# Performance work log

Hardware: AMD Instinct MI355X
Metric: run time of the kernel (lower is better)

## Reference

```python
import jax, jax.numpy as jnp
import numpy as np

B, V, T, F, H = 32, 16, 64, 64, 512
NBINS = 36  # 360 / delta (delta_cog = delta_rb = 10)
OUT = 4     # output_size


def setup_inputs() -> dict:
    key = jax.random.key(0)
    ks = jax.random.split(key, 12)
    s = 1.0 / np.sqrt(H)
    return {
        'sequence': jax.random.normal(ks[0], (B, V, T, F), jnp.float32),
        'dist_matrix': jax.random.uniform(ks[1], (B, V, T, V), jnp.float32),
        'rb_matrix': jax.random.randint(ks[2], (B, V, T, V), 0, NBINS).astype(jnp.int32),
        'cog_matrix': jax.random.randint(ks[3], (B, V, T, V), 0, NBINS).astype(jnp.int32),
        'seq_mask': jnp.ones((B, V, T), jnp.float32),
        'maxval': jax.random.uniform(ks[4], (B, F), jnp.float32) + 1.0,
        'minval': jax.random.uniform(ks[5], (B, F), jnp.float32),
        # per-vessel LSTMCell params (PyTorch gate order i,f,g,o stacked along 4H)
        'W_ih': jax.random.normal(ks[6], (V, 4 * H, F), jnp.float32) * s,
        'W_hh': jax.random.normal(ks[7], (V, 4 * H, H), jnp.float32) * s,
        'b_ih': jnp.zeros((V, 4 * H), jnp.float32),
        'b_hh': jnp.zeros((V, 4 * H), jnp.float32),
        # hardwired attention domain table [360/delta_cog, 360/delta_rb]
        'domain': jax.random.normal(ks[8], (NBINS, NBINS), jnp.float32),
        # per-vessel softAttention linear (2H -> H)
        'soft_W': jax.random.normal(ks[9], (V, H, 2 * H), jnp.float32) * s,
        'soft_b': jnp.zeros((V, H), jnp.float32),
        # shared output linear (H -> F)
        'out_W': jax.random.normal(ks[10], (F, H), jnp.float32) * s,
        'out_b': jnp.zeros((F,), jnp.float32),
    }


def _forward(sequence, dist_matrix, rb_matrix, cog_matrix, seq_mask, maxval, minval,
             W_ih, W_hh, b_ih, b_hh, domain, soft_W, soft_b, out_W, out_b):
    B_, V_, T_, F_ = sequence.shape
    H_ = W_hh.shape[-1]

    def hardwired(h, r, d, m, cg):
        # h: [B,V,H]; r,d,cg: [B,V,V]; m: [B,V]
        mul1 = m[:, :, None] * m[:, None, :]
        mul2 = domain[cg, r]
        w = jax.nn.relu(mul2 - d) * mul1
        w = w / jax.lax.stop_gradient(jnp.max(w))  # torch: weights /= weights.data.max()
        return jnp.einsum('bvw,bwh->bvh', w, h)

    def lstm_step(x, h, c):
        # vectorized over V independent LSTMCells
        g = (jnp.einsum('bvf,vgf->bvg', x, W_ih)
             + jnp.einsum('bvh,vgh->bvg', h, W_hh) + b_ih + b_hh)
        i, f, gg, o = jnp.split(g, 4, axis=-1)
        c_new = jax.nn.sigmoid(f) * c + jax.nn.sigmoid(i) * jnp.tanh(gg)
        h_new = jax.nn.sigmoid(o) * jnp.tanh(c_new)
        return h_new, c_new

    h0 = jnp.zeros((B_, V_, H_), sequence.dtype)
    c0 = jnp.zeros((B_, V_, H_), sequence.dtype)
    xs = (jnp.moveaxis(sequence, 2, 0), jnp.moveaxis(rb_matrix, 2, 0),
          jnp.moveaxis(dist_matrix, 2, 0), jnp.moveaxis(seq_mask, 2, 0),
          jnp.moveaxis(cog_matrix, 2, 0))

    def enc_step(carry, xt):
        h, c = carry
        x, r, d, m, cg = xt
        wh = hardwired(h, r, d, m, cg)
        h, c = lstm_step(x, wh, c)
        return (h, c), h

    (h, c), enc = jax.lax.scan(enc_step, (h0, c0), xs)
    enc = jnp.moveaxis(enc, 0, 2)  # encodedInput [B,V,T,H]

    # decoder, prediction step i=0 (prediction_length=1)
    wh = hardwired(h, rb_matrix[:, :, -1], dist_matrix[:, :, -1],
                   seq_mask[:, :, -1], cog_matrix[:, :, -1])
    # get_previous_sequence: denormalize under no_grad
    prev = jax.lax.stop_gradient(
        sequence[:, :, -1] * (maxval - minval)[:, None, :] + minval[:, None, :])
    h, c = lstm_step(prev, wh, c)

    # per-vessel softAttention
    score = jnp.einsum('bvth,bvh->bvt', enc, h)
    alpha = jax.nn.softmax(score * seq_mask, axis=-1)
    ctx = jnp.einsum('bvt,bvth->bvh', alpha, enc)
    # faithful to torch.stack((ctx, h)).view(B, 2H) memory-reinterpret per vessel
    z = jnp.moveaxis(jnp.stack([ctx, h], axis=0), 2, 0).reshape(V_, B_, 2 * H_)
    h = jnp.moveaxis(
        jnp.tanh(jnp.einsum('vbk,vhk->vbh', z, soft_W) + soft_b[:, None, :]), 0, 1)

    out = jax.nn.relu(jnp.einsum('bvh,fh->bvf', h, out_W) + out_b)
    return out[:, :, None, :OUT]  # [B, V, prediction_length=1, output_size]


def reference(sequence, dist_matrix, rb_matrix, cog_matrix, seq_mask, maxval, minval,
              W_ih, W_hh, b_ih, b_hh, domain, soft_W, soft_b, out_W, out_b,
              maxVessels=V):
    return _forward(sequence, dist_matrix, rb_matrix, cog_matrix, seq_mask,
                    maxval, minval, W_ih, W_hh, b_ih, b_hh, domain,
                    soft_W, soft_b, out_W, out_b)
```

## Files before the change

### kernel.cpp

```cpp
#include <hip/hip_runtime.h>
#include <math.h>

#define B 32
#define V 16
#define T 64
#define F 64
#define H 512
#define NB 36
#define G4H 2048

typedef unsigned short u16;
typedef unsigned long long ull;
typedef __attribute__((ext_vector_type(8))) short bf16x8;
typedef __attribute__((ext_vector_type(4))) float f32x4;

#define OFF_H0     0
#define OFF_H1     262144
#define OFF_C      524288
#define OFF_CNT    786432
#define OFF_WALL   819200
#define OFF_CTX    819200
#define OFF_HSOFT  1081344
#define OFF_WMAX   1343488
#define OFF_WHSTG  1343552
#define OFF_SEQSTG 1605696
#define OFF_WSTG   2670656
#define OFF_ENC    12107840

#define WHP 262144
#define WLDS_BYTES 147456

__device__ __forceinline__ float sigmoidf_(float x) { return 1.0f / (1.0f + __expf(-x)); }

__device__ __forceinline__ u16 f2bf(float f) {
    union { float f; unsigned u; } x; x.f = f;
    unsigned r = x.u + 0x7FFF + ((x.u >> 16) & 1);
    return (u16)(r >> 16);
}
__device__ __forceinline__ float bf2f(u16 u) {
    union { unsigned i; float f; } x; x.i = ((unsigned)u) << 16;
    return x.f;
}
__device__ __forceinline__ f32x4 mfma16(bf16x8 a, bf16x8 b, f32x4 c) {
    return __builtin_amdgcn_mfma_f32_16x16x32_bf16(a, b, c, 0, 0, 0);
}
__device__ __forceinline__ bf16x8 mk_bf16x8(ull lo, ull hi) {
    union { ull u[2]; bf16x8 v; } x; x.u[0] = lo; x.u[1] = hi; return x.v;
}
__device__ __forceinline__ bf16x8 mk_bf16x8q(uint4 q) {
    union { uint4 q; bf16x8 v; } x; x.q = q; return x.v;
}

__device__ __forceinline__ ull ld_agent(const ull* p) {
    return __hip_atomic_load((ull*)p, __ATOMIC_RELAXED, __HIP_MEMORY_SCOPE_AGENT);
}
__device__ __forceinline__ void st_agent(ull* p, ull x) {
    __hip_atomic_store(p, x, __ATOMIC_RELAXED, __HIP_MEMORY_SCOPE_AGENT);
}
__device__ __forceinline__ void st_agent_f(float* p, float x) {
    __hip_atomic_store(p, x, __ATOMIC_RELAXED, __HIP_MEMORY_SCOPE_AGENT);
}
__device__ __forceinline__ void st_agent_u16(u16* p, u16 x) {
    __hip_atomic_store(p, x, __ATOMIC_RELAXED, __HIP_MEMORY_SCOPE_AGENT);
}
__device__ __forceinline__ void st_agent_u32(unsigned* p, unsigned x) {
    __hip_atomic_store(p, x, __ATOMIC_RELAXED, __HIP_MEMORY_SCOPE_AGENT);
}
__device__ __forceinline__ unsigned ld_agent_u32(const unsigned* p) {
    return __hip_atomic_load((unsigned*)p, __ATOMIC_RELAXED, __HIP_MEMORY_SCOPE_AGENT);
}

#define NZB 3200
#define NHW 64
#define NWC 4608
#define NSS 1040
__global__ __launch_bounds__(256) void k_prep(
    float* __restrict__ ws,
    const float* __restrict__ dist, const int* __restrict__ rb,
    const int* __restrict__ cog, const float* __restrict__ mask,
    const float* __restrict__ domain, float* __restrict__ w_all,
    float* __restrict__ wmax_all,
    const float* __restrict__ W_ih, const float* __restrict__ W_hh,
    u16* __restrict__ Wstg,
    const float* __restrict__ seq, const float* __restrict__ maxval,
    const float* __restrict__ minval, u16* __restrict__ seqstg) {
    __shared__ float red[256];
    int bid = blockIdx.x;
    int tid = threadIdx.x;

    if (bid < NZB) {
        ws[bid * 256 + tid] = 0.0f;
        return;
    }
    if (bid < NZB + NHW) {
        int t = bid - NZB;
        float lmax = 0.0f;
        for (int idx = tid; idx < B * V * V; idx += 256) {
            int b = idx >> 8;
            int rem = idx & 255;
            int i = rem >> 4, j = rem & 15;
            int base = ((b * V + i) * T + t) * V + j;
            float val = domain[cog[base] * NB + rb[base]] - dist[base];
            val = val > 0.0f ? val : 0.0f;
            val *= mask[(b * V + i) * T + t] * mask[(b * V + j) * T + t];
            w_all[t * (B * V * V) + idx] = val;
            lmax = fmaxf(lmax, val);
        }
        red[tid] = lmax;
        __syncthreads();
        for (int s = 128; s > 0; s >>= 1) {
            if (tid < s) red[tid] = fmaxf(red[tid], red[tid + s]);
            __syncthreads();
        }
        if (tid == 0) wmax_all[t] = red[0];
        return;
    }
    if (bid < NZB + NHW + NWC) {
        int idx = bid - (NZB + NHW);
        int v = idx / 288, hk = (idx / 18) & 15, ks = idx % 18;
#pragma unroll
        for (int s = 0; s < 2; ++s) {
            int slot = tid + s * 256;
            int nt = slot >> 6, lane = slot & 63;
            int g = nt >> 1, hh = nt & 1;
            int col = g * H + hk * 32 + hh * 16 + (lane & 15);
            int k = ks * 32 + ((lane >> 4) << 3);
            const float* src = (k < F) ? &W_ih[(v * G4H + col) * F + k]
                                       : &W_hh[(v * G4H + col) * H + (k - F)];
            float4 x0 = *(const float4*)src;
            float4 x1 = *(const float4*)(src + 4);
            union { u16 u[8]; uint4 q; } pk;
            pk.u[0] = f2bf(x0.x); pk.u[1] = f2bf(x0.y); pk.u[2] = f2bf(x0.z); pk.u[3] = f2bf(x0.w);
            pk.u[4] = f2bf(x1.x); pk.u[5] = f2bf(x1.y); pk.u[6] = f2bf(x1.z); pk.u[7] = f2bf(x1.w);
            *(uint4*)&Wstg[(size_t)((((v * 16 + hk) * 18 + ks) * 8 + nt) * 64 + lane) * 8] = pk.q;
        }
        return;
    }
    {
        int idx = bid - (NZB + NHW + NWC);
        int v = idx / 65, t = idx % 65;
        int mt = tid >> 7, ks = (tid >> 6) & 1, lane = tid & 63;
        int b = mt * 16 + (lane & 15);
        int f = ks * 32 + ((lane >> 4) << 3);
        union { u16 u[8]; uint4 q; } pk;
        if (t < T) {
            const float* sp = &seq[((b * V + v) * T + t) * F + f];
            float4 x0 = *(const float4*)sp, x1 = *(const float4*)(sp + 4);
            pk.u[0] = f2bf(x0.x); pk.u[1] = f2bf(x0.y); pk.u[2] = f2bf(x0.z); pk.u[3] = f2bf(x0.w);
            pk.u[4] = f2bf(x1.x); pk.u[5] = f2bf(x1.y); pk.u[6] = f2bf(x1.z); pk.u[7] = f2bf(x1.w);
        } else {
            const float* sp = &seq[((b * V + v) * T + (T - 1)) * F + f];
            float4 x0 = *(const float4*)sp, x1 = *(const float4*)(sp + 4);
            float4 mx0 = *(const float4*)&maxval[b * F + f], mx1 = *(const float4*)&maxval[b * F + f + 4];
            float4 mn0 = *(const float4*)&minval[b * F + f], mn1 = *(const float4*)&minval[b * F + f + 4];
            pk.u[0] = f2bf(x0.x * (mx0.x - mn0.x) + mn0.x);
            pk.u[1] = f2bf(x0.y * (mx0.y - mn0.y) + mn0.y);
            pk.u[2] = f2bf(x0.z * (mx0.z - mn0.z) + mn0.z);
            pk.u[3] = f2bf(x0.w * (mx0.w - mn0.w) + mn0.w);
            pk.u[4] = f2bf(x1.x * (mx1.x - mn1.x) + mn1.x);
            pk.u[5] = f2bf(x1.y * (mx1.y - mn1.y) + mn1.y);
            pk.u[6] = f2bf(x1.z * (mx1.z - mn1.z) + mn1.z);
            pk.u[7] = f2bf(x1.w * (mx1.w - mn1.w) + mn1.w);
        }
        *(uint4*)&seqstg[(((size_t)(t * 16 + v)) * 4 + mt * 2 + ks) * 512 + lane * 8] = pk.q;
    }
}

__global__ __launch_bounds__(256) void k_main(
    const u16* __restrict__ seqstg, const u16* __restrict__ Wstg,
    const float* __restrict__ w_all, const float* __restrict__ wmax_all,
    const float* __restrict__ b_ih, const float* __restrict__ b_hh,
    float* __restrict__ h0buf, float* __restrict__ h1buf,
    float* __restrict__ c, u16* __restrict__ enc, u16* __restrict__ whstg,
    unsigned* __restrict__ bar,
    const float* __restrict__ mask, const float* __restrict__ soft_W,
    const float* __restrict__ soft_b, const float* __restrict__ out_W,
    const float* __restrict__ out_b, float* __restrict__ ctx,
    float* __restrict__ hsoft, float* __restrict__ out) {
    extern __shared__ u16 Wlds[];
    __shared__ float hs[H];
    __shared__ float scal[2 * T];
    __shared__ float sA[32][36];
    __shared__ float sW2[32][36];

    int bid = blockIdx.x;
    int v = bid & 15, hk = bid >> 4;
    int tid = threadIdx.x;

    {
        const uint4* wsrc = (const uint4*)(Wstg + (size_t)((v * 16 + hk) * 18) * 4096);
        uint4* wdst = (uint4*)Wlds;
        for (int i = tid; i < 9216; i += 256) wdst[i] = wsrc[i];
    }

    int lane = tid & 63, wvi = tid >> 6;
    int mtw = wvi & 1, hh = wvi >> 1;
    int col = hk * 32 + hh * 16 + (lane & 15);
    int q4 = (lane >> 4) << 2;
    float bi = b_ih[v * G4H + col] + b_hh[v * G4H + col];
    float bf_ = b_ih[v * G4H + H + col] + b_hh[v * G4H + H + col];
    float bg_ = b_ih[v * G4H + 2 * H + col] + b_hh[v * G4H + 2 * H + col];
    float bo = b_ih[v * G4H + 3 * H + col] + b_hh[v * G4H + 3 * H + col];

    unsigned* aslot = bar + (v * 16 + hk) * 16;
    unsigned* bslot = bar + (256 + hk * 16 + v) * 16;
    unsigned* apoll = bar + (v * 16 + (tid & 15)) * 16;
    unsigned* bpoll = bar + (256 + hk * 16 + (tid & 15)) * 16;

    int a_b = tid >> 3;
    int a_cq = tid & 7;
    const int wh_idx = ((((v * 2 + (a_b >> 4)) * 16 + hk) * 64 +
                         (((a_cq >> 1) << 4) + (a_b & 15))) * 8 + (a_cq & 1) * 4);

    __syncthreads();

    for (int t = 0; t <= T; ++t) {
        int par = t & 1;
        int tm = t < T ? t : (T - 1);
        const float* hin = (t & 1) ? h0buf : h1buf;
        float* hout = (t & 1) ? h1buf : h0buf;

        uint4 s0 = *(const uint4*)&seqstg[(((size_t)(t * 16 + v)) * 4 + mtw * 2 + 0) * 512 + lane * 8];
        uint4 s1 = *(const uint4*)&seqstg[(((size_t)(t * 16 + v)) * 4 + mtw * 2 + 1) * 512 + lane * 8];
        float inv = 1.0f / wmax_all[tm];
        const float* wrow = &w_all[(size_t)tm * (B * V * V) + (a_b * V + v) * V];
        float4 wr0 = *(const float4*)(wrow);
        float4 wr1 = *(const float4*)(wrow + 4);
        float4 wr2 = *(const float4*)(wrow + 8);
        float4 wr3 = *(const float4*)(wrow + 12);
        float cprev[4];
#pragma unroll
        for (int r = 0; r < 4; ++r)
            cprev[r] = c[((mtw * 16 + q4 + r) * V + v) * H + col];

        f32x4 acc[4];
        acc[0][0] = bi;  acc[0][1] = bi;  acc[0][2] = bi;  acc[0][3] = bi;
        acc[1][0] = bf_; acc[1][1] = bf_; acc[1][2] = bf_; acc[1][3] = bf_;
        acc[2][0] = bg_; acc[2][1] = bg_; acc[2][2] = bg_; acc[2][3] = bg_;
        acc[3][0] = bo;  acc[3][1] = bo;  acc[3][2] = bo;  acc[3][3] = bo;
        {
            bf16x8 a0f = mk_bf16x8q(s0);
            bf16x8 a1f = mk_bf16x8q(s1);
#pragma unroll
            for (int g = 0; g < 4; ++g)
                acc[g] = mfma16(a0f, *(const bf16x8*)&Wlds[(0 * 8 + (g * 2 + hh)) * 512 + lane * 8], acc[g]);
#pragma unroll
            for (int g = 0; g < 4; ++g)
                acc[g] = mfma16(a1f, *(const bf16x8*)&Wlds[(1 * 8 + (g * 2 + hh)) * 512 + lane * 8], acc[g]);
        }

        if (t > 0) {
            if (tid < 16) {
                while (ld_agent_u32(bpoll) < (unsigned)t) __builtin_amdgcn_s_sleep(1);
            }
            __syncthreads();
        }

        {
            const ull* hb = (const ull*)&hin[(a_b * V) * H + hk * 32 + a_cq * 4];
            float a0 = 0.f, a1 = 0.f, a2 = 0.f, a3 = 0.f;
            const float wj[16] = {wr0.x, wr0.y, wr0.z, wr0.w, wr1.x, wr1.y, wr1.z, wr1.w,
                                  wr2.x, wr2.y, wr2.z, wr2.w, wr3.x, wr3.y, wr3.z, wr3.w};
#pragma unroll
            for (int j = 0; j < 16; ++j) {
                ull lo = ld_agent(hb + (size_t)j * (H / 2));
                ull hi = ld_agent(hb + (size_t)j * (H / 2) + 1);
                union { ull u; float f[2]; } u0, u1;
                u0.u = lo; u1.u = hi;
                a0 = fmaf(wj[j], u0.f[0], a0);
                a1 = fmaf(wj[j], u0.f[1], a1);
                a2 = fmaf(wj[j], u1.f[0], a2);
                a3 = fmaf(wj[j], u1.f[1], a3);
            }
            union { u16 u[4]; ull q; } pk;
            pk.u[0] = f2bf(a0 * inv); pk.u[1] = f2bf(a1 * inv);
            pk.u[2] = f2bf(a2 * inv); pk.u[3] = f2bf(a3 * inv);
            st_agent((ull*)&whstg[par * WHP + wh_idx], pk.q);
        }
        __syncthreads();
        if (tid == 0) st_agent_u32(aslot, (unsigned)(t + 1));

        if (tid < 16) {
            while (ld_agent_u32(apoll) < (unsigned)(t + 1)) __builtin_amdgcn_s_sleep(1);
        }
        __syncthreads();

        bf16x8 afr[16];
#pragma unroll
        for (int ksw = 0; ksw < 16; ++ksw) {
            const ull* src = (const ull*)&whstg[par * WHP + (((v * 2 + mtw) * 16 + ksw) * 64 + lane) * 8];
            ull lo = ld_agent(src), hi = ld_agent(src + 1);
            afr[ksw] = mk_bf16x8(lo, hi);
        }
#pragma unroll
        for (int ks = 0; ks < 16; ++ks) {
#pragma unroll
            for (int g = 0; g < 4; ++g) {
                bf16x8 wfr = *(const bf16x8*)&Wlds[((ks + 2) * 8 + (g * 2 + hh)) * 512 + lane * 8];
                acc[g] = mfma16(afr[ks], wfr, acc[g]);
            }
        }

        float cnv[4], hnv[4];
#pragma unroll
        for (int r = 0; r < 4; ++r) {
            float gi = acc[0][r];
            float gf = acc[1][r];
            float gg = acc[2][r];
            float go = acc[3][r];
            cnv[r] = sigmoidf_(gf) * cprev[r] + sigmoidf_(gi) * tanhf(gg);
            hnv[r] = sigmoidf_(go) * tanhf(cnv[r]);
            int b = mtw * 16 + q4 + r;
            st_agent_f(&hout[(b * V + v) * H + col], hnv[r]);
        }
        if (t < T) {
            __syncthreads();
            if (tid == 0) st_agent_u32(bslot, (unsigned)(t + 1));
        }

#pragma unroll
        for (int r = 0; r < 4; ++r) {
            int b = mtw * 16 + q4 + r;
            c[(b * V + v) * H + col] = cnv[r];
            if (t < T) st_agent_u16(&enc[((size_t)(b * V + v) * T + t) * H + col], f2bf(hnv[r]));
        }
    }

    __syncthreads();
    if (tid == 0) st_agent_u32(bar + (512 + bid) * 16, 1u);
    {
        const unsigned* rs = bar + (512 + tid) * 16;
        while (ld_agent_u32(rs) < 1u) __builtin_amdgcn_s_sleep(1);
    }
    __syncthreads();

    for (int u = 0; u < 2; ++u) {
        int ab = (bid >> 4) + u * 16;
        int av = bid & 15;
        const u16* encb = enc + ((size_t)(ab * V + av) * T) * H;
        {
            ull x = ld_agent((const ull*)(h0buf + (ab * V + av) * H) + tid);
            union { ull u; float f[2]; } q; q.u = x;
            hs[tid * 2] = q.f[0]; hs[tid * 2 + 1] = q.f[1];
        }
        __syncthreads();
        for (int tt = wvi; tt < T; tt += 4) {
            const ull* ep = (const ull*)(encb + tt * H + lane * 8);
            ull lo = ld_agent(ep), hi = ld_agent(ep + 1);
            union { ull u; u16 s[4]; } x0, x1; x0.u = lo; x1.u = hi;
            const float* hq = &hs[lane * 8];
            float p = bf2f(x0.s[0]) * hq[0] + bf2f(x0.s[1]) * hq[1]
                    + bf2f(x0.s[2]) * hq[2] + bf2f(x0.s[3]) * hq[3]
                    + bf2f(x1.s[0]) * hq[4] + bf2f(x1.s[1]) * hq[5]
                    + bf2f(x1.s[2]) * hq[6] + bf2f(x1.s[3]) * hq[7];
            for (int off = 32; off; off >>= 1) p += __shfl_down(p, off, 64);
            if (lane == 0) scal[tt] = p;
        }
        __syncthreads();
        if (tid < 64) {
            float m_t = mask[(ab * V + av) * T + tid];
            float s = scal[tid] * m_t;
            float mx = s;
            for (int off = 32; off; off >>= 1) mx = fmaxf(mx, __shfl_xor(mx, off, 64));
            float e = __expf(s - mx);
            float sum = e;
            for (int off = 32; off; off >>= 1) sum += __shfl_xor(sum, off, 64);
            scal[T + tid] = e / sum;
        }
        __syncthreads();
        if (tid < 128) {
            float a0 = 0.f, a1 = 0.f, a2 = 0.f, a3 = 0.f;
            for (int tt = 0; tt < T; ++tt) {
                ull x = ld_agent((const ull*)(encb + tt * H + tid * 4));
                union { ull u; u16 s[4]; } q; q.u = x;
                float al = scal[T + tt];
                a0 = fmaf(al, bf2f(q.s[0]), a0);
                a1 = fmaf(al, bf2f(q.s[1]), a1);
                a2 = fmaf(al, bf2f(q.s[2]), a2);
                a3 = fmaf(al, bf2f(q.s[3]), a3);
            }
            float* cp = ctx + (ab * V + av) * H + tid * 4;
            union { float f[2]; ull u; } q0, q1;
            q0.f[0] = a0; q0.f[1] = a1; q1.f[0] = a2; q1.f[1] = a3;
            st_agent((ull*)cp, q0.u);
            st_agent((ull*)cp + 1, q1.u);
        }
        __syncthreads();
    }
    __syncthreads();
    if (tid == 0) st_agent_u32(bar + (768 + bid) * 16, 1u);

    {
        int sv = bid & 15;
        int h0 = (bid >> 4) * 32;
        if (tid < 16) {
            const unsigned* cs = bar + (768 + tid * 16 + sv) * 16;
            while (ld_agent_u32(cs) < 1u) __builtin_amdgcn_s_sleep(1);
        }
        __syncthreads();

        int cg = tid & 31, rg = tid >> 5;
        float* sAf = &sA[0][0];
        float* sWf = &sW2[0][0];
        float accs[4] = {0.f, 0.f, 0.f, 0.f};
        int arow = tid >> 3, akq = tid & 7;
        float4 areg, wreg;
        {
            int k = akq * 4;
            const float* src = (arow < 16) ? ctx : h0buf;
            int bsrc = 2 * (arow & 15) + (k >= H ? 1 : 0);
            const float* sp = &src[(bsrc * V + sv) * H + (k & (H - 1))];
            ull l0 = ld_agent((const ull*)sp), l1 = ld_agent((const ull*)sp + 1);
            union { ull u[2]; float4 f; } q; q.u[0] = l0; q.u[1] = l1;
            areg = q.f;
            wreg = *(const float4*)&soft_W[(sv * H + h0 + arow) * (2 * H) + k];
        }
        for (int kc = 0; kc < 2 * H; kc += 32) {
            __syncthreads();
            *(float4*)&sAf[arow * 36 + akq * 4] = areg;
            *(float4*)&sWf[arow * 36 + akq * 4] = wreg;
            __syncthreads();
            if (kc + 32 < 2 * H) {
                int k = kc + 32 + akq * 4;
                const float* src = (arow < 16) ? ctx : h0buf;
                int bsrc = 2 * (arow & 15) + (k >= H ? 1 : 0);
                const float* sp = &src[(bsrc * V + sv) * H + (k & (H - 1))];
                ull l0 = ld_agent((const ull*)sp), l1 = ld_agent((const ull*)sp + 1);
                union { ull u[2]; float4 f; } q; q.u[0] = l0; q.u[1] = l1;
                areg = q.f;
                wreg = *(const float4*)&soft_W[(sv * H + h0 + arow) * (2 * H) + kc + 32 + akq * 4];
            }
#pragma unroll
            for (int k4 = 0; k4 < 8; ++k4) {
                float4 wv = *(const float4*)&sWf[cg * 36 + k4 * 4];
                float4 a0 = *(const float4*)&sAf[(rg * 4 + 0) * 36 + k4 * 4];
                float4 a1 = *(const float4*)&sAf[(rg * 4 + 1) * 36 + k4 * 4];
                float4 a2 = *(const float4*)&sAf[(rg * 4 + 2) * 36 + k4 * 4];
                float4 a3 = *(const float4*)&sAf[(rg * 4 + 3) * 36 + k4 * 4];
                accs[0] += a0.x * wv.x + a0.y * wv.y + a0.z * wv.z + a0.w * wv.w;
                accs[1] += a1.x * wv.x + a1.y * wv.y + a1.z * wv.z + a1.w * wv.w;
                accs[2] += a2.x * wv.x + a2.y * wv.y + a2.z * wv.z + a2.w * wv.w;
                accs[3] += a3.x * wv.x + a3.y * wv.y + a3.z * wv.z + a3.w * wv.w;
            }
        }
        float bb = soft_b[sv * H + h0 + cg];
#pragma unroll
        for (int r = 0; r < 4; ++r) {
            int row = rg * 4 + r;
            st_agent_f(&hsoft[(row * V + sv) * H + h0 + cg], tanhf(accs[r] + bb));
        }
    }
    __syncthreads();
    if (tid == 0) st_agent_u32(bar + (1024 + bid) * 16, 1u);

    {
        int ov = bid & 15;
        if (tid < 16) {
            const unsigned* ss = bar + (1024 + tid * 16 + ov) * 16;
            while (ld_agent_u32(ss) < 1u) __builtin_amdgcn_s_sleep(1);
        }
        __syncthreads();
        if (wvi < 2) {
            int ob = (bid >> 4) + wvi * 16;
            const float* hbp = hsoft + (ob * V + ov) * H + lane * 8;
            ull q0 = ld_agent((const ull*)hbp);
            ull q1 = ld_agent((const ull*)hbp + 1);
            ull q2 = ld_agent((const ull*)hbp + 2);
            ull q3 = ld_agent((const ull*)hbp + 3);
            union { ull u[4]; float f[8]; } hv;
            hv.u[0] = q0; hv.u[1] = q1; hv.u[2] = q2; hv.u[3] = q3;
            float p[4] = {0.f, 0.f, 0.f, 0.f};
#pragma unroll
            for (int o = 0; o < 4; ++o) {
                const float* wp = &out_W[o * H + lane * 8];
#pragma unroll
                for (int j = 0; j < 8; ++j) p[o] += hv.f[j] * wp[j];
            }
#pragma unroll
            for (int o = 0; o < 4; ++o) {
                float s = p[o];
                for (int off = 32; off; off >>= 1) s += __shfl_down(s, off, 64);
                if (lane == 0) {
                    float val = s + out_b[o];
                    out[(ob * V + ov) * 4 + o] = val > 0.0f ? val : 0.0f;
                }
            }
        }
    }
}

extern "C" void kernel_launch(void* const* d_in, const int* in_sizes, int n_in,
                              void* d_out, int out_size, void* d_ws, size_t ws_size,
                              hipStream_t stream) {
    const float* seq = (const float*)d_in[0];
    const float* dist = (const float*)d_in[1];
    const int* rb = (const int*)d_in[2];
    const int* cog = (const int*)d_in[3];
    const float* mask = (const float*)d_in[4];
    const float* maxval = (const float*)d_in[5];
    const float* minval = (const float*)d_in[6];
    const float* W_ih = (const float*)d_in[7];
    const float* W_hh = (const float*)d_in[8];
    const float* b_ih = (const float*)d_in[9];
    const float* b_hh = (const float*)d_in[10];
    const float* domain = (const float*)d_in[11];
    const float* soft_W = (const float*)d_in[12];
    const float* soft_b = (const float*)d_in[13];
    const float* out_W = (const float*)d_in[14];
    const float* out_b = (const float*)d_in[15];

    float* ws = (float*)d_ws;
    float* h0buf = ws + OFF_H0;
    float* h1buf = ws + OFF_H1;
    float* c = ws + OFF_C;
    unsigned* bar = (unsigned*)(ws + OFF_CNT);
    float* w_all = ws + OFF_WALL;
    float* ctx = ws + OFF_CTX;
    float* hsoft = ws + OFF_HSOFT;
    float* wmax_all = ws + OFF_WMAX;
    u16* whstg = (u16*)(ws + OFF_WHSTG);
    u16* seqstg = (u16*)(ws + OFF_SEQSTG);
    u16* Wstg = (u16*)(ws + OFF_WSTG);
    u16* enc = (u16*)(ws + OFF_ENC);

    (void)hipFuncSetAttribute((const void*)k_main,
                              hipFuncAttributeMaxDynamicSharedMemorySize, WLDS_BYTES);

    k_prep<<<NZB + NHW + NWC + NSS, 256, 0, stream>>>(
        ws, dist, rb, cog, mask, domain, w_all, wmax_all,
        W_ih, W_hh, Wstg, seq, maxval, minval, seqstg);

    k_main<<<256, 256, WLDS_BYTES, stream>>>(seqstg, Wstg, w_all, wmax_all,
                                             b_ih, b_hh, h0buf, h1buf, c, enc,
                                             whstg, bar, mask, soft_W, soft_b,
                                             out_W, out_b, ctx, hsoft,
                                             (float*)d_out);
}
```

Baseline: 856.6 us.

## Split persistent kernel into recurrence and tail kernels; coalesce weight staging via LDS

The monolithic persistent kernel is split into a recurrence kernel and a separate tail kernel for attention and output. This replaces the grid-wide barrier and the agent-scope atomic loads and stores of enc and h with a kernel boundary and plain loads. The weight-staging prep now uses 256 blocks, each loading full rows coalesced into an LDS tile and transposing there, instead of 4608 blocks doing scattered loads. The cost is an extra kernel launch and fewer, heavier prep blocks.

```diff
diff --git a/kernel.cpp b/kernel.cpp
--- a/kernel.cpp
+++ b/kernel.cpp
@@ -60,9 +60,6 @@
 __device__ __forceinline__ void st_agent_f(float* p, float x) {
     __hip_atomic_store(p, x, __ATOMIC_RELAXED, __HIP_MEMORY_SCOPE_AGENT);
 }
-__device__ __forceinline__ void st_agent_u16(u16* p, u16 x) {
-    __hip_atomic_store(p, x, __ATOMIC_RELAXED, __HIP_MEMORY_SCOPE_AGENT);
-}
 __device__ __forceinline__ void st_agent_u32(unsigned* p, unsigned x) {
     __hip_atomic_store(p, x, __ATOMIC_RELAXED, __HIP_MEMORY_SCOPE_AGENT);
 }
@@ -72,7 +69,7 @@
 
 #define NZB 3200
 #define NHW 64
-#define NWC 4608
+#define NWC 256
 #define NSS 1040
 __global__ __launch_bounds__(256) void k_prep(
     float* __restrict__ ws,
@@ -85,6 +82,7 @@
     const float* __restrict__ seq, const float* __restrict__ maxval,
     const float* __restrict__ minval, u16* __restrict__ seqstg) {
     __shared__ float red[256];
+    __shared__ float tile[128 * 36];
     int bid = blockIdx.x;
     int tid = threadIdx.x;
 
@@ -117,22 +115,41 @@
     }
     if (bid < NZB + NHW + NWC) {
         int idx = bid - (NZB + NHW);
-        int v = idx / 288, hk = (idx / 18) & 15, ks = idx % 18;
-#pragma unroll
-        for (int s = 0; s < 2; ++s) {
-            int slot = tid + s * 256;
-            int nt = slot >> 6, lane = slot & 63;
-            int g = nt >> 1, hh = nt & 1;
-            int col = g * H + hk * 32 + hh * 16 + (lane & 15);
-            int k = ks * 32 + ((lane >> 4) << 3);
-            const float* src = (k < F) ? &W_ih[(v * G4H + col) * F + k]
-                                       : &W_hh[(v * G4H + col) * H + (k - F)];
-            float4 x0 = *(const float4*)src;
-            float4 x1 = *(const float4*)(src + 4);
-            union { u16 u[8]; uint4 q; } pk;
-            pk.u[0] = f2bf(x0.x); pk.u[1] = f2bf(x0.y); pk.u[2] = f2bf(x0.z); pk.u[3] = f2bf(x0.w);
-            pk.u[4] = f2bf(x1.x); pk.u[5] = f2bf(x1.y); pk.u[6] = f2bf(x1.z); pk.u[7] = f2bf(x1.w);
-            *(uint4*)&Wstg[(size_t)((((v * 16 + hk) * 18 + ks) * 8 + nt) * 64 + lane) * 8] = pk.q;
+        int v = idx >> 4, hk = idx & 15;
+        int lr = tid >> 1, half = tid & 1;
+        int lg = lr >> 5, rloc = lr & 31;
+        int srcrow = v * G4H + lg * 512 + hk * 32 + rloc;
+        for (int ks = 0; ks < 18; ++ks) {
+            const float* srcp = (ks < 2)
+                ? &W_ih[srcrow * F + ks * 32 + half * 16]
+                : &W_hh[srcrow * H + (ks * 32 - 64) + half * 16];
+            float4 x0 = *(const float4*)srcp;
+            float4 x1 = *(const float4*)(srcp + 4);
+            float4 x2 = *(const float4*)(srcp + 8);
+            float4 x3 = *(const float4*)(srcp + 12);
+            __syncthreads();
+            float* dst = &tile[lr * 36 + half * 16];
+            *(float4*)(dst + 0) = x0;
+            *(float4*)(dst + 4) = x1;
+            *(float4*)(dst + 8) = x2;
+            *(float4*)(dst + 12) = x3;
+            __syncthreads();
+#pragma unroll
+            for (int s = 0; s < 2; ++s) {
+                int slot = tid + s * 256;
+                int nt = slot >> 6, lane = slot & 63;
+                int g = nt >> 1, hh = nt & 1;
+                int ldsrow = g * 32 + hh * 16 + (lane & 15);
+                int kloc = (lane >> 4) << 3;
+                float4 y0 = *(const float4*)&tile[ldsrow * 36 + kloc];
+                float4 y1 = *(const float4*)&tile[ldsrow * 36 + kloc + 4];
+                union { u16 u[8]; uint4 q; } pk;
+                pk.u[0] = f2bf(y0.x); pk.u[1] = f2bf(y0.y);
+                pk.u[2] = f2bf(y0.z); pk.u[3] = f2bf(y0.w);
+                pk.u[4] = f2bf(y1.x); pk.u[5] = f2bf(y1.y);
+                pk.u[6] = f2bf(y1.z); pk.u[7] = f2bf(y1.w);
+                *(uint4*)&Wstg[(size_t)((((v * 16 + hk) * 18 + ks) * 8 + nt) * 64 + lane) * 8] = pk.q;
+            }
         }
         return;
     }
@@ -166,22 +183,14 @@
     }
 }
 
-__global__ __launch_bounds__(256) void k_main(
+__global__ __launch_bounds__(256) void k_recur(
     const u16* __restrict__ seqstg, const u16* __restrict__ Wstg,
     const float* __restrict__ w_all, const float* __restrict__ wmax_all,
     const float* __restrict__ b_ih, const float* __restrict__ b_hh,
     float* __restrict__ h0buf, float* __restrict__ h1buf,
     float* __restrict__ c, u16* __restrict__ enc, u16* __restrict__ whstg,
-    unsigned* __restrict__ bar,
-    const float* __restrict__ mask, const float* __restrict__ soft_W,
-    const float* __restrict__ soft_b, const float* __restrict__ out_W,
-    const float* __restrict__ out_b, float* __restrict__ ctx,
-    float* __restrict__ hsoft, float* __restrict__ out) {
+    unsigned* __restrict__ bar) {
     extern __shared__ u16 Wlds[];
-    __shared__ float hs[H];
-    __shared__ float scal[2 * T];
-    __shared__ float sA[32][36];
-    __shared__ float sW2[32][36];
 
     int bid = blockIdx.x;
     int v = bid & 15, hk = bid >> 4;
@@ -322,37 +331,44 @@
         for (int r = 0; r < 4; ++r) {
             int b = mtw * 16 + q4 + r;
             c[(b * V + v) * H + col] = cnv[r];
-            if (t < T) st_agent_u16(&enc[((size_t)(b * V + v) * T + t) * H + col], f2bf(hnv[r]));
-        }
-    }
-
-    __syncthreads();
-    if (tid == 0) st_agent_u32(bar + (512 + bid) * 16, 1u);
-    {
-        const unsigned* rs = bar + (512 + tid) * 16;
-        while (ld_agent_u32(rs) < 1u) __builtin_amdgcn_s_sleep(1);
-    }
-    __syncthreads();
+            if (t < T) enc[((size_t)(b * V + v) * T + t) * H + col] = f2bf(hnv[r]);
+        }
+    }
+}
+
+__global__ __launch_bounds__(256) void k_tail(
+    const u16* __restrict__ enc, const float* __restrict__ hfin,
+    const float* __restrict__ mask, const float* __restrict__ soft_W,
+    const float* __restrict__ soft_b, const float* __restrict__ out_W,
+    const float* __restrict__ out_b, float* __restrict__ ctx,
+    float* __restrict__ hsoft, float* __restrict__ out,
+    unsigned* __restrict__ bar) {
+    __shared__ float hs[H];
+    __shared__ float scal[2 * T];
+    __shared__ float sA[32][36];
+    __shared__ float sW2[32][36];
+
+    int bid = blockIdx.x;
+    int tid = threadIdx.x;
+    int lane = tid & 63, wvi = tid >> 6;
 
     for (int u = 0; u < 2; ++u) {
         int ab = (bid >> 4) + u * 16;
         int av = bid & 15;
         const u16* encb = enc + ((size_t)(ab * V + av) * T) * H;
         {
-            ull x = ld_agent((const ull*)(h0buf + (ab * V + av) * H) + tid);
-            union { ull u; float f[2]; } q; q.u = x;
-            hs[tid * 2] = q.f[0]; hs[tid * 2 + 1] = q.f[1];
+            float2 q = *(const float2*)(hfin + (ab * V + av) * H + tid * 2);
+            hs[tid * 2] = q.x; hs[tid * 2 + 1] = q.y;
         }
         __syncthreads();
         for (int tt = wvi; tt < T; tt += 4) {
-            const ull* ep = (const ull*)(encb + tt * H + lane * 8);
-            ull lo = ld_agent(ep), hi = ld_agent(ep + 1);
-            union { ull u; u16 s[4]; } x0, x1; x0.u = lo; x1.u = hi;
+            uint4 x = *(const uint4*)(encb + tt * H + lane * 8);
+            union { uint4 q; u16 s[8]; } e; e.q = x;
             const float* hq = &hs[lane * 8];
-            float p = bf2f(x0.s[0]) * hq[0] + bf2f(x0.s[1]) * hq[1]
-                    + bf2f(x0.s[2]) * hq[2] + bf2f(x0.s[3]) * hq[3]
-                    + bf2f(x1.s[0]) * hq[4] + bf2f(x1.s[1]) * hq[5]
-                    + bf2f(x1.s[2]) * hq[6] + bf2f(x1.s[3]) * hq[7];
+            float p = bf2f(e.s[0]) * hq[0] + bf2f(e.s[1]) * hq[1]
+                    + bf2f(e.s[2]) * hq[2] + bf2f(e.s[3]) * hq[3]
+                    + bf2f(e.s[4]) * hq[4] + bf2f(e.s[5]) * hq[5]
+                    + bf2f(e.s[6]) * hq[6] + bf2f(e.s[7]) * hq[7];
             for (int off = 32; off; off >>= 1) p += __shfl_down(p, off, 64);
             if (lane == 0) scal[tt] = p;
         }
@@ -371,7 +387,7 @@
         if (tid < 128) {
             float a0 = 0.f, a1 = 0.f, a2 = 0.f, a3 = 0.f;
             for (int tt = 0; tt < T; ++tt) {
-                ull x = ld_agent((const ull*)(encb + tt * H + tid * 4));
+                ull x = *(const ull*)(encb + tt * H + tid * 4);
                 union { ull u; u16 s[4]; } q; q.u = x;
                 float al = scal[T + tt];
                 a0 = fmaf(al, bf2f(q.s[0]), a0);
@@ -407,7 +423,7 @@
         float4 areg, wreg;
         {
             int k = akq * 4;
-            const float* src = (arow < 16) ? ctx : h0buf;
+            const float* src = (arow < 16) ? ctx : hfin;
             int bsrc = 2 * (arow & 15) + (k >= H ? 1 : 0);
             const float* sp = &src[(bsrc * V + sv) * H + (k & (H - 1))];
             ull l0 = ld_agent((const ull*)sp), l1 = ld_agent((const ull*)sp + 1);
@@ -422,7 +438,7 @@
             __syncthreads();
             if (kc + 32 < 2 * H) {
                 int k = kc + 32 + akq * 4;
-                const float* src = (arow < 16) ? ctx : h0buf;
+                const float* src = (arow < 16) ? ctx : hfin;
                 int bsrc = 2 * (arow & 15) + (k >= H ? 1 : 0);
                 const float* sp = &src[(bsrc * V + sv) * H + (k & (H - 1))];
                 ull l0 = ld_agent((const ull*)sp), l1 = ld_agent((const ull*)sp + 1);
@@ -523,16 +539,18 @@
     u16* Wstg = (u16*)(ws + OFF_WSTG);
     u16* enc = (u16*)(ws + OFF_ENC);
 
-    (void)hipFuncSetAttribute((const void*)k_main,
+    (void)hipFuncSetAttribute((const void*)k_recur,
                               hipFuncAttributeMaxDynamicSharedMemorySize, WLDS_BYTES);
 
     k_prep<<<NZB + NHW + NWC + NSS, 256, 0, stream>>>(
         ws, dist, rb, cog, mask, domain, w_all, wmax_all,
         W_ih, W_hh, Wstg, seq, maxval, minval, seqstg);
 
-    k_main<<<256, 256, WLDS_BYTES, stream>>>(seqstg, Wstg, w_all, wmax_all,
-                                             b_ih, b_hh, h0buf, h1buf, c, enc,
-                                             whstg, bar, mask, soft_W, soft_b,
-                                             out_W, out_b, ctx, hsoft,
-                                             (float*)d_out);
-}
+    k_recur<<<256, 256, WLDS_BYTES, stream>>>(seqstg, Wstg, w_all, wmax_all,
+                                              b_ih, b_hh, h0buf, h1buf, c, enc,
+                                              whstg, bar);
+
+    k_tail<<<256, 256, 0, stream>>>(enc, h0buf, mask, soft_W, soft_b,
+                                    out_W, out_b, ctx, hsoft,
+                                    (float*)d_out, bar);
+}
```

After: 710.0 us. 1.21x faster.
